# Kernel optimization log

Measured on AMD Instinct MI355X. Metric: run time of the kernel, lower is better.

## Reference

```python
import jax, jax.numpy as jnp
import numpy as np
import math

B, SV, ST, D, H = 16, 1024, 512, 768, 8
DH = D // H


def layernorm(x, g, b, eps=1e-5):
    m = jnp.mean(x, axis=-1, keepdims=True)
    v = jnp.var(x, axis=-1, keepdims=True)
    return (x - m) / jnp.sqrt(v + eps) * g + b


def setup_inputs() -> dict:
    key = jax.random.key(0)
    ks = jax.random.split(key, 12)
    s = 1.0 / math.sqrt(D)
    inp = {
        "visual_features": jax.random.normal(ks[0], (B, SV, D), jnp.float32),
        "text_features": jax.random.normal(ks[1], (B, ST, D), jnp.float32),
        "visual_mask": jnp.ones((B, SV), jnp.int32),
        "text_mask": jnp.ones((B, ST), jnp.int32),
        "Wq": jax.random.normal(ks[2], (D, D), jnp.float32) * s,
        "bq": jnp.zeros((D,), jnp.float32),
        "Wk": jax.random.normal(ks[3], (D, D), jnp.float32) * s,
        "bk": jnp.zeros((D,), jnp.float32),
        "Wv": jax.random.normal(ks[4], (D, D), jnp.float32) * s,
        "bv": jnp.zeros((D,), jnp.float32),
        "Wo": jax.random.normal(ks[5], (D, D), jnp.float32) * s,
        "bo": jnp.zeros((D,), jnp.float32),
        "ln1_g": jnp.ones((D,), jnp.float32),
        "ln1_b": jnp.zeros((D,), jnp.float32),
        "Wf": jax.random.normal(ks[6], (2 * D, D), jnp.float32) * (1.0 / math.sqrt(2 * D)),
        "bf": jnp.zeros((D,), jnp.float32),
        "ln2_g": jnp.ones((D,), jnp.float32),
        "ln2_b": jnp.zeros((D,), jnp.float32),
    }
    return inp


def _heads(x):
    b, s, _ = x.shape
    return x.reshape(b, s, H, DH)


def _cross_attn(q_feats, kv_feats, kv_mask, Wq, bq, Wk, bk, Wv, bv):
    # q_feats: [B,Sq,D], kv_feats: [B,Sk,D], kv_mask: [B,Sk] or None
    q = _heads(q_feats @ Wq + bq)   # [B,Sq,H,DH]
    k = _heads(kv_feats @ Wk + bk)  # [B,Sk,H,DH]
    v = _heads(kv_feats @ Wv + bv)
    scores = jnp.einsum('bqhd,bkhd->bhqk', q, k) / math.sqrt(DH)
    if kv_mask is not None:
        scores = jnp.where(kv_mask[:, None, None, :] == 0, -jnp.inf, scores)
    attn = jax.nn.softmax(scores, axis=-1)  # dropout is identity in eval
    out = jnp.einsum('bhqk,bkhd->bqhd', attn, v)
    return out.reshape(q_feats.shape[0], q_feats.shape[1], D)


def reference(visual_features, text_features, visual_mask, text_mask,
              Wq, bq, Wk, bk, Wv, bv, Wo, bo, ln1_g, ln1_b,
              Wf, bf, ln2_g, ln2_b):
    # visual queries attend to text
    v2t = _cross_attn(visual_features, text_features, text_mask, Wq, bq, Wk, bk, Wv, bv)
    # text queries attend to visual
    t2v = _cross_attn(text_features, visual_features, visual_mask, Wq, bq, Wk, bk, Wv, bv)
    attended_visual = layernorm(visual_features + (v2t @ Wo + bo), ln1_g, ln1_b)
    attended_text = layernorm(text_features + (t2v @ Wo + bo), ln1_g, ln1_b)
    # masked mean pooling
    vm = visual_mask[:, :, None].astype(jnp.float32)
    pooled_v = (attended_visual * vm).sum(1) / vm.sum(1)
    tm = text_mask[:, :, None].astype(jnp.float32)
    pooled_t = (attended_text * tm).sum(1) / tm.sum(1)
    fused = jnp.concatenate([pooled_v, pooled_t], axis=-1) @ Wf + bf
    fused = layernorm(fused, ln2_g, ln2_b)  # dropout identity in eval
    return fused
```

## Files before the change

kernel.cpp:

```cpp
#include <hip/hip_runtime.h>

typedef __bf16 bf16x8 __attribute__((ext_vector_type(8)));
typedef __bf16 bf16x4v __attribute__((ext_vector_type(4)));
typedef short s16x4 __attribute__((ext_vector_type(4)));
typedef float f32x4 __attribute__((ext_vector_type(4)));
typedef unsigned short u16;
typedef unsigned int u32;
typedef u16 u16x8 __attribute__((ext_vector_type(8)));
typedef u16 u16x4 __attribute__((ext_vector_type(4)));


__device__ __forceinline__ u16 f2bf(float f) {
    u32 u = __builtin_bit_cast(u32, f);
    u32 r = u + 0x7FFFu + ((u >> 16) & 1u);
    return (u16)(r >> 16);
}

__device__ __forceinline__ float bf2f(u16 b) {
    u32 u = ((u32)b) << 16;
    return __builtin_bit_cast(float, u);
}

__device__ __forceinline__ f32x4 mfma16(bf16x8 a, bf16x8 b, f32x4 c) {
    return __builtin_amdgcn_mfma_f32_16x16x32_bf16(a, b, c, 0, 0, 0);
}

__device__ __forceinline__ f32x4 mfma16k16(bf16x4v a, bf16x4v b, f32x4 c) {
#if __has_builtin(__builtin_amdgcn_mfma_f32_16x16x16_bf16)
    return __builtin_amdgcn_mfma_f32_16x16x16_bf16(a, b, c, 0, 0, 0);
#elif __has_builtin(__builtin_amdgcn_mfma_f32_16x16x16bf16_1k)
    return __builtin_amdgcn_mfma_f32_16x16x16bf16_1k(
        __builtin_bit_cast(s16x4, a), __builtin_bit_cast(s16x4, b), c, 0, 0, 0);
#else
    f32x4 d;
    asm volatile("v_mfma_f32_16x16x16_bf16 %0, %1, %2, %3"
                 : "=v"(d) : "v"(a), "v"(b), "v"(c));
    return d;
#endif
}

#define GLOAD_LDS16(g, l) __builtin_amdgcn_global_load_lds( \
    (__attribute__((address_space(1))) void*)(g), \
    (__attribute__((address_space(3))) void*)(l), 16, 0, 0)


__global__ __launch_bounds__(256) void k_cvt_x(const float* __restrict__ vf,
                                               const float* __restrict__ tf,
                                               u16* __restrict__ X, int nvis4) {
    int i = blockIdx.x * 256 + threadIdx.x;
    f32x4 v = (i < nvis4) ? ((const f32x4*)vf)[i] : ((const f32x4*)tf)[i - nvis4];
    u16x4 o = { f2bf(v[0]), f2bf(v[1]), f2bf(v[2]), f2bf(v[3]) };
    ((u16x4*)X)[i] = o;
}

__global__ __launch_bounds__(256) void k_transpose(const float* __restrict__ src,
                                                   u16* __restrict__ dst,
                                                   int K0, int N0) {
    __shared__ float t[64][65];
    int ntx = N0 >> 6;
    int k0 = (blockIdx.x / ntx) << 6, n0 = (blockIdx.x % ntx) << 6;
    int c = threadIdx.x & 63, rr = threadIdx.x >> 6;
#pragma unroll
    for (int q = 0; q < 16; q++) {
        int r = q * 4 + rr;
        t[r][c] = src[(size_t)(k0 + r) * N0 + n0 + c];
    }
    __syncthreads();
#pragma unroll
    for (int q = 0; q < 16; q++) {
        int r = q * 4 + rr;
        dst[(size_t)(n0 + r) * K0 + k0 + c] = f2bf(t[c][r]);
    }
}

__global__ __launch_bounds__(256) void k_bias(const float* __restrict__ bq,
                                              const float* __restrict__ bk,
                                              const float* __restrict__ bv,
                                              float* __restrict__ bqkv) {
    int n = blockIdx.x * 256 + threadIdx.x;
    if (n < 2304) {
        const float* s = (n < 768) ? bq : ((n < 1536) ? bk : bv);
        int r = (n < 768) ? n : ((n < 1536) ? n - 768 : n - 1536);
        bqkv[n] = s[r];
    }
}

__global__ __launch_bounds__(256) void k_zero(float* __restrict__ p) {
    p[blockIdx.x * 256 + threadIdx.x] = 0.f;
}

template <bool OUT_BF16, bool ADD_RES, bool SPLIT_VT>
__global__ __launch_bounds__(256) void k_gemm(const u16* __restrict__ A,
                                              const u16* __restrict__ Bt,
                                              const float* __restrict__ bias,
                                              const float* __restrict__ resA,
                                              const float* __restrict__ resB,
                                              void* __restrict__ Cout,
                                              int Ndim, int Kdim, int mvisL,
                                              u16* __restrict__ VtGp, int Rtot) {
    __shared__ alignas(16) u16 sA[2][128 * 32];
    __shared__ alignas(16) u16 sB[2][128 * 32];
    const int tid = threadIdx.x, wid = tid >> 6, lane = tid & 63;
    const int nwg = gridDim.x;
    const int wg = (blockIdx.x & 7) * (nwg >> 3) + (blockIdx.x >> 3);
    const int ntiles = Ndim >> 7;
    const int mt = wg / ntiles, nt = wg - mt * ntiles;
    const int m0 = mt << 7, n0 = nt << 7;
    const int wm = wid >> 1, wn = wid & 1;
    f32x4 acc[4][4] = {};

    const int r0 = tid >> 2, p0 = tid & 3;
    const int r1 = 64 + r0;
    const u16* ga0 = A + (size_t)(m0 + r0) * Kdim + p0 * 8;
    const u16* ga1 = A + (size_t)(m0 + r1) * Kdim + p0 * 8;
    const u16* gb0 = Bt + (size_t)(n0 + r0) * Kdim + p0 * 8;
    const u16* gb1 = Bt + (size_t)(n0 + r1) * Kdim + p0 * 8;
    const int loff0 = wid * 512;
    const int loff1 = 2048 + wid * 512;

    const int arow = (wm << 6) + (lane & 15);
    const int brow = (wn << 6) + (lane & 15);
    const int kg = (lane >> 4) * 8;

    auto stage = [&](int kt, int pb) {
        GLOAD_LDS16(ga0 + kt, &sA[pb][loff0]);
        GLOAD_LDS16(ga1 + kt, &sA[pb][loff1]);
        GLOAD_LDS16(gb0 + kt, &sB[pb][loff0]);
        GLOAD_LDS16(gb1 + kt, &sB[pb][loff1]);
    };

    const int niter = Kdim >> 5;
    stage(0, 0);
    for (int it = 0; it < niter; ++it) {
        const int cur = it & 1;
        __syncthreads();
        if (it + 1 < niter) stage((it + 1) << 5, cur ^ 1);
        bf16x8 av[4], bw[4];
#pragma unroll
        for (int i = 0; i < 4; i++) av[i] = *(const bf16x8*)&sA[cur][(arow + i * 16) * 32 + kg];
#pragma unroll
        for (int j = 0; j < 4; j++) bw[j] = *(const bf16x8*)&sB[cur][(brow + j * 16) * 32 + kg];
#pragma unroll
        for (int i = 0; i < 4; i++)
#pragma unroll
            for (int j = 0; j < 4; j++) acc[i][j] = mfma16(av[i], bw[j], acc[i][j]);
    }

    const int col0 = n0 + (wn << 6) + (lane & 15);
    const int rowb = m0 + (wm << 6) + ((lane >> 4) << 2);
    float bvals[4];
#pragma unroll
    for (int j = 0; j < 4; j++) bvals[j] = bias[col0 + j * 16];

    if constexpr (SPLIT_VT) {
        if (n0 >= 1536) {
            const int vcol0 = col0 - 1536;
#pragma unroll
            for (int i = 0; i < 4; i++) {
#pragma unroll
                for (int j = 0; j < 4; j++) {
                    u16x4 o4;
#pragma unroll
                    for (int rg = 0; rg < 4; rg++) o4[rg] = f2bf(acc[i][j][rg] + bvals[j]);
                    *(u16x4*)&VtGp[(size_t)(vcol0 + j * 16) * Rtot + rowb + i * 16] = o4;
                }
            }
            return;
        }
    }

#pragma unroll
    for (int i = 0; i < 4; i++) {
#pragma unroll
        for (int rg = 0; rg < 4; rg++) {
            const int row = rowb + i * 16 + rg;
            const float* rp = nullptr;
            if constexpr (ADD_RES)
                rp = (row < mvisL) ? resA + (size_t)row * 768
                                   : resB + (size_t)(row - mvisL) * 768;
#pragma unroll
            for (int j = 0; j < 4; j++) {
                const int col = col0 + j * 16;
                float v = acc[i][j][rg] + bvals[j];
                if constexpr (ADD_RES) v += rp[col];
                if constexpr (OUT_BF16)
                    ((u16*)Cout)[(size_t)row * Ndim + col] = f2bf(v);
                else
                    ((float*)Cout)[(size_t)row * Ndim + col] = v;
            }
        }
    }
}

__global__ __launch_bounds__(512) void k_attn(const u16* __restrict__ qkv,
                                              const u16* __restrict__ VtG,
                                              const int* __restrict__ vmaskc,
                                              const int* __restrict__ tmaskc,
                                              u16* __restrict__ attn, int CHn, int Rtot) {
    __shared__ alignas(16) u16 Kl[2][128 * 128];
    __shared__ alignas(16) u16 Vt[2][96 * 128];
    __shared__ float mk[2][128];

    const int bx = blockIdx.x;
    int b, h, qbase, kbase, nqt, ntl;
    const int* mask;
    const int vcap = CHn * 8;
    if (bx < vcap) {
        b = bx >> 3; h = bx & 7;
        qbase = b << 10; kbase = (CHn << 10) + (b << 9);
        mask = tmaskc + (b << 9); nqt = 4; ntl = 2;
    } else {
        const int bx2 = bx - vcap;
        b = bx2 >> 3; h = bx2 & 7;
        qbase = (CHn << 10) + (b << 9); kbase = b << 10;
        mask = vmaskc + (b << 10); nqt = 2; ntl = 3;
    }
    const int ntile = 1 << ntl;
    const int nsteps = nqt << ntl;
    const int tid = threadIdx.x, wid = tid >> 6, lane = tid & 63;
    const int l15 = lane & 15, l4 = lane >> 4;
    const float scale = 0.10206207261596577f;

    int koff[3];
#pragma unroll
    for (int kk = 0; kk < 3; kk++) koff[kk] = ((kk * 4 + l4) ^ (l15 & 7)) << 3;

    auto kt_of = [&](int s) {
        const int qt = s >> ntl, ktr = s & (ntile - 1);
        return (qt & 1) ? (ntile - 1 - ktr) : ktr;
    };
    auto stage = [&](int kt, int pb) {
#pragma unroll
        for (int it = 0; it < 4; ++it) {
            const int cb = it * 512 + (wid << 6);
            const int c = cb + lane;
            const int r = c >> 4, s8 = c & 15;
            const int k8 = s8 ^ (r & 7);
            const u16* src = qkv + (size_t)(kbase + (kt << 7) + r) * 2304 + 768 + h * 96
                             + (k8 < 12 ? k8 * 8 : 0);
            GLOAD_LDS16(src, &Kl[pb][(size_t)cb * 8]);
        }
#pragma unroll
        for (int it = 0; it < 3; ++it) {
            const int cb = it * 512 + (wid << 6);
            const int c = cb + lane;
            const int d = c >> 4, s8 = c & 15;
            const int k8 = s8 ^ (d & 7);
            const u16* src = VtG + (size_t)(h * 96 + d) * Rtot + kbase + (kt << 7) + k8 * 8;
            GLOAD_LDS16(src, &Vt[pb][(size_t)cb * 8]);
        }
        if (tid < 128) mk[pb][tid] = mask[(kt << 7) + tid] ? 0.f : -1e30f;
    };

    stage(kt_of(0), 0);
    int s = 0;
    for (int qt = 0; qt < nqt; ++qt) {
        bf16x8 aq[2][3];
#pragma unroll
        for (int qs = 0; qs < 2; ++qs) {
            const int qr = qbase + (qt << 8) + (wid << 5) + qs * 16 + l15;
#pragma unroll
            for (int kk = 0; kk < 3; kk++) {
                bf16x8 tq = *(const bf16x8*)&qkv[(size_t)qr * 2304 + h * 96 + kk * 32 + l4 * 8];
#pragma unroll
                for (int e = 0; e < 8; e++) tq[e] = (__bf16)((float)tq[e] * scale);
                aq[qs][kk] = tq;
            }
        }
        f32x4 o[2][6] = {};
        float mrunS[2] = {-1e30f, -1e30f};
        float lrunS[2] = {0.f, 0.f};

        for (int ktr = 0; ktr < ntile; ++ktr, ++s) {
            const int cur = s & 1;
            __syncthreads();
            if (s + 1 < nsteps) stage(kt_of(s + 1), cur ^ 1);

            f32x4 sc[2][8];
#pragma unroll
            for (int j = 0; j < 8; j++) {
                const int rbase = (j * 16 + l15) * 128;
                bf16x8 bk[3];
#pragma unroll
                for (int kk = 0; kk < 3; kk++)
                    bk[kk] = *(const bf16x8*)&Kl[cur][rbase + koff[kk]];
#pragma unroll
                for (int qs = 0; qs < 2; ++qs) {
                    f32x4 cj = {0.f, 0.f, 0.f, 0.f};
#pragma unroll
                    for (int kk = 0; kk < 3; kk++) cj = mfma16(bk[kk], aq[qs][kk], cj);
                    sc[qs][j] = cj;
                }
            }

            bf16x4v pb[2][8];
#pragma unroll
            for (int qs = 0; qs < 2; ++qs) {
                float tm = -1e30f;
#pragma unroll
                for (int j = 0; j < 8; j++) {
                    f32x4 m4 = *(const f32x4*)&mk[cur][j * 16 + (l4 << 2)];
#pragma unroll
                    for (int rg = 0; rg < 4; rg++) {
                        float v = sc[qs][j][rg] + m4[rg];
                        sc[qs][j][rg] = v;
                        tm = fmaxf(tm, v);
                    }
                }
                tm = fmaxf(tm, __shfl_xor(tm, 16));
                tm = fmaxf(tm, __shfl_xor(tm, 32));
                const int need = (tm > mrunS[qs] + 8.f) ? 1 : 0;
                if (__any(need)) {
                    float mn = fmaxf(mrunS[qs], tm);
                    float corrS = __expf(mrunS[qs] - mn);
                    mrunS[qs] = mn;
                    lrunS[qs] *= corrS;
                    float cr[4];
#pragma unroll
                    for (int rg = 0; rg < 4; rg++) cr[rg] = __shfl(corrS, (l4 << 2) + rg);
#pragma unroll
                    for (int j6 = 0; j6 < 6; j6++)
#pragma unroll
                        for (int rg = 0; rg < 4; rg++) o[qs][j6][rg] *= cr[rg];
                }
                float ts = 0.f;
#pragma unroll
                for (int j = 0; j < 8; j++) {
                    bf16x4v pq;
#pragma unroll
                    for (int rg = 0; rg < 4; rg++) {
                        float p = __expf(sc[qs][j][rg] - mrunS[qs]);
                        ts += p;
                        pq[rg] = (__bf16)p;
                    }
                    pb[qs][j] = pq;
                }
                ts += __shfl_xor(ts, 16);
                ts += __shfl_xor(ts, 32);
                lrunS[qs] += ts;
            }

#pragma unroll
            for (int j = 0; j < 8; j++) {
                const int slotb = 2 * j + (l4 >> 1);
                const int intra = (l4 & 1) << 2;
#pragma unroll
                for (int j6 = 0; j6 < 6; j6++) {
                    const int d = j6 * 16 + l15;
                    bf16x4v bv = *(const bf16x4v*)&Vt[cur][d * 128 +
                                     ((slotb ^ (l15 & 7)) << 3) + intra];
                    o[0][j6] = mfma16k16(pb[0][j], bv, o[0][j6]);
                    o[1][j6] = mfma16k16(pb[1][j], bv, o[1][j6]);
                }
            }
        }

#pragma unroll
        for (int qs = 0; qs < 2; ++qs) {
            const float invS = 1.f / lrunS[qs];
            float inv[4];
#pragma unroll
            for (int rg = 0; rg < 4; rg++) inv[rg] = __shfl(invS, (l4 << 2) + rg);
            const size_t orow = (size_t)(qbase + (qt << 8) + (wid << 5) + qs * 16);
#pragma unroll
            for (int j6 = 0; j6 < 6; j6++)
#pragma unroll
                for (int rg = 0; rg < 4; rg++)
                    attn[(orow + l4 * 4 + rg) * 768 + h * 96 + j6 * 16 + l15] =
                        f2bf(o[qs][j6][rg] * inv[rg]);
        }
    }
}

__global__ __launch_bounds__(256) void k_ln_pool(const u16* __restrict__ X,
                                                 const int* __restrict__ vmaskc,
                                                 const int* __restrict__ tmaskc,
                                                 const float* __restrict__ g,
                                                 const float* __restrict__ bb,
                                                 float* __restrict__ pooled,
                                                 int mvisL, int bg0) {
    __shared__ float pool[768];
    const int tid = threadIdx.x, wid = tid >> 6, lane = tid & 63;
    const int row0 = blockIdx.x << 5;
    const bool vis = row0 < mvisL;
    const int* mask = vis ? vmaskc : tmaskc;
    const int mbase = vis ? 0 : mvisL;
    const int bl = vis ? (row0 >> 10) : ((row0 - mvisL) >> 9);
    float* pout = pooled + (vis ? 0 : 12288) + (size_t)(bg0 + bl) * 768;

    float gv[12], bv2[12];
#pragma unroll
    for (int k = 0; k < 12; k++) { gv[k] = g[lane + k * 64]; bv2[k] = bb[lane + k * 64]; }
    float acc[12] = {};
    for (int rr = 0; rr < 8; ++rr) {
        const int row = row0 + (wid << 3) + rr;
        const u16* x = X + (size_t)row * 768;
        float xs[12], sm = 0.f, s2 = 0.f;
#pragma unroll
        for (int k = 0; k < 12; k++) {
            float tv = bf2f(x[lane + k * 64]);
            xs[k] = tv; sm += tv; s2 += tv * tv;
        }
#pragma unroll
        for (int d = 1; d < 64; d <<= 1) { sm += __shfl_xor(sm, d); s2 += __shfl_xor(s2, d); }
        const float mean = sm * (1.f / 768.f);
        const float rstd = rsqrtf(s2 * (1.f / 768.f) - mean * mean + 1e-5f);
        const float mv = (float)mask[row - mbase];
#pragma unroll
        for (int k = 0; k < 12; k++) acc[k] += ((xs[k] - mean) * rstd * gv[k] + bv2[k]) * mv;
    }
    pool[tid] = 0.f; pool[tid + 256] = 0.f; pool[tid + 512] = 0.f;
    __syncthreads();
#pragma unroll
    for (int k = 0; k < 12; k++) atomicAdd(&pool[lane + k * 64], acc[k]);
    __syncthreads();
    atomicAdd(&pout[tid], pool[tid]);
    atomicAdd(&pout[tid + 256], pool[tid + 256]);
    atomicAdd(&pout[tid + 512], pool[tid + 512]);
}

__device__ __forceinline__ float blk_sum(float v, volatile float* tmp) {
#pragma unroll
    for (int d = 1; d < 64; d <<= 1) v += __shfl_xor(v, d);
    __syncthreads();
    if ((threadIdx.x & 63) == 0) tmp[threadIdx.x >> 6] = v;
    __syncthreads();
    return tmp[0] + tmp[1] + tmp[2] + tmp[3];
}

__global__ __launch_bounds__(256) void k_final(const float* __restrict__ pooled,
                                               const int* __restrict__ vmask,
                                               const int* __restrict__ tmask,
                                               const float* __restrict__ Wf,
                                               const float* __restrict__ bfv,
                                               const float* __restrict__ g2,
                                               const float* __restrict__ b2,
                                               float* __restrict__ out) {
    __shared__ float sh[1536];
    __shared__ float red[4];
    const int b = blockIdx.x, tid = threadIdx.x;
    float cv = 0.f, ct = 0.f;
    for (int i = tid; i < 1024; i += 256) cv += (float)vmask[(b << 10) + i];
    for (int i = tid; i < 512; i += 256) ct += (float)tmask[(b << 9) + i];
    cv = blk_sum(cv, red);
    ct = blk_sum(ct, red);
    const float iv = 1.f / cv, itv = 1.f / ct;
#pragma unroll
    for (int k = 0; k < 3; k++) {
        int j = tid + (k << 8);
        sh[j] = pooled[b * 768 + j] * iv;
        sh[768 + j] = pooled[12288 + b * 768 + j] * itv;
    }
    __syncthreads();
    float f0 = bfv[tid], f1 = bfv[tid + 256], f2 = bfv[tid + 512];
    for (int i = 0; i < 1536; i++) {
        const float pv = sh[i];
        const float* w = Wf + (size_t)i * 768;
        f0 += pv * w[tid];
        f1 += pv * w[tid + 256];
        f2 += pv * w[tid + 512];
    }
    float sm = blk_sum(f0 + f1 + f2, red);
    float s2 = blk_sum(f0 * f0 + f1 * f1 + f2 * f2, red);
    const float mean = sm * (1.f / 768.f);
    const float rstd = rsqrtf(s2 * (1.f / 768.f) - mean * mean + 1e-5f);
    out[b * 768 + tid] = (f0 - mean) * rstd * g2[tid] + b2[tid];
    out[b * 768 + tid + 256] = (f1 - mean) * rstd * g2[tid + 256] + b2[tid + 256];
    out[b * 768 + tid + 512] = (f2 - mean) * rstd * g2[tid + 512] + b2[tid + 512];
}

extern "C" void kernel_launch(void* const* d_in, const int* in_sizes, int n_in,
                              void* d_out, int out_size, void* d_ws, size_t ws_size,
                              hipStream_t stream) {
    (void)in_sizes; (void)n_in; (void)out_size;
    const float* vf = (const float*)d_in[0];
    const float* tf = (const float*)d_in[1];
    const int* vmask = (const int*)d_in[2];
    const int* tmask = (const int*)d_in[3];
    const float* Wq = (const float*)d_in[4];
    const float* bq = (const float*)d_in[5];
    const float* Wk = (const float*)d_in[6];
    const float* bk = (const float*)d_in[7];
    const float* Wv = (const float*)d_in[8];
    const float* bv = (const float*)d_in[9];
    const float* Wo = (const float*)d_in[10];
    const float* bo = (const float*)d_in[11];
    const float* g1 = (const float*)d_in[12];
    const float* b1 = (const float*)d_in[13];
    const float* Wf = (const float*)d_in[14];
    const float* bfv = (const float*)d_in[15];
    const float* g2 = (const float*)d_in[16];
    const float* b2 = (const float*)d_in[17];
    float* outp = (float*)d_out;

    int CH = 16;
    while (CH > 1 && 4826112ull + (size_t)CH * 11796480ull > ws_size) CH >>= 1;
    const int NC = 16 / CH;
    const int Rtot = CH * 1536;

    char* ws = (char*)d_ws;
    u16*   wsW      = (u16*)(ws);
    u16*   wsWo     = (u16*)(ws + 3538944);
    float* wsBqkv   = (float*)(ws + 4718592);
    float* wsPooled = (float*)(ws + 4727808);
    u16*   wsX      = (u16*)(ws + 4826112);
    char*  qkvBase  = ws + 4826112 + (size_t)CH * 2359296;
    u16*   wsQKV    = (u16*)qkvBase;
    u16*   wsOproj  = (u16*)qkvBase;
    u16*   wsVtG    = (u16*)(qkvBase + (size_t)CH * 7077888);
    u16*   wsAttn   = wsX;

    k_transpose<<<dim3(144), dim3(256), 0, stream>>>(Wq, wsW, 768, 768);
    k_transpose<<<dim3(144), dim3(256), 0, stream>>>(Wk, wsW + 589824, 768, 768);
    k_transpose<<<dim3(144), dim3(256), 0, stream>>>(Wv, wsW + 1179648, 768, 768);
    k_transpose<<<dim3(144), dim3(256), 0, stream>>>(Wo, wsWo, 768, 768);
    k_bias<<<dim3(9), dim3(256), 0, stream>>>(bq, bk, bv, wsBqkv);
    k_zero<<<dim3(96), dim3(256), 0, stream>>>(wsPooled);

    for (int c = 0; c < NC; ++c) {
        const float* vfc = vf + (size_t)c * CH * 1024 * 768;
        const float* tfc = tf + (size_t)c * CH * 512 * 768;
        const int* vmc = vmask + c * CH * 1024;
        const int* tmc = tmask + c * CH * 512;

        k_cvt_x<<<dim3(CH * 1152), dim3(256), 0, stream>>>(vfc, tfc, wsX, CH * 196608);

        k_gemm<true, false, true><<<dim3(CH * 216), dim3(256), 0, stream>>>(
            wsX, wsW, wsBqkv, nullptr, nullptr, (void*)wsQKV, 2304, 768, 0, wsVtG, Rtot);

        k_attn<<<dim3(CH * 16), dim3(512), 0, stream>>>(
            wsQKV, wsVtG, vmc, tmc, wsAttn, CH, Rtot);

        k_gemm<true, true, false><<<dim3(CH * 72), dim3(256), 0, stream>>>(
            wsAttn, wsWo, bo, vfc, tfc, (void*)wsOproj, 768, 768, CH * 1024, nullptr, 0);

        k_ln_pool<<<dim3(CH * 48), dim3(256), 0, stream>>>(
            wsOproj, vmc, tmc, g1, b1, wsPooled, CH * 1024, c * CH);
    }

    k_final<<<dim3(16), dim3(256), 0, stream>>>(wsPooled, vmask, tmask, Wf, bfv, g2, b2, outp);
}
```

Measured before the change: 433.9 us.

## Enlarge GEMM tile to 256x128 with 512 threads and split final matvec across waves

The GEMM kernel moves from 128x128 tiles with 256 threads to 256x128 tiles with 512 threads (8 waves). The grid is halved and the A tile is staged as two 128-row halves, so each B tile is reused across twice as many rows. When the grid size is not a multiple of 8, the XCD-swizzle remapping is skipped. In the final fusion kernel, the 1536-long reduction is split across the 4 waves and combined through shared memory. The bigger tiles double LDS use and produce fewer workgroups, which may lower occupancy or leave the machine under-filled for small chunks.

```diff
diff --git a/kernel.cpp b/kernel.cpp
--- a/kernel.cpp
+++ b/kernel.cpp
@@ -90,7 +90,7 @@
 }
 
 template <bool OUT_BF16, bool ADD_RES, bool SPLIT_VT>
-__global__ __launch_bounds__(256) void k_gemm(const u16* __restrict__ A,
+__global__ __launch_bounds__(512) void k_gemm(const u16* __restrict__ A,
                                               const u16* __restrict__ Bt,
                                               const float* __restrict__ bias,
                                               const float* __restrict__ resA,
@@ -98,36 +98,35 @@
                                               void* __restrict__ Cout,
                                               int Ndim, int Kdim, int mvisL,
                                               u16* __restrict__ VtGp, int Rtot) {
-    __shared__ alignas(16) u16 sA[2][128 * 32];
+    __shared__ alignas(16) u16 sA[2][256 * 32];
     __shared__ alignas(16) u16 sB[2][128 * 32];
     const int tid = threadIdx.x, wid = tid >> 6, lane = tid & 63;
     const int nwg = gridDim.x;
-    const int wg = (blockIdx.x & 7) * (nwg >> 3) + (blockIdx.x >> 3);
+    const int wg = (nwg & 7) ? (int)blockIdx.x
+                             : ((blockIdx.x & 7) * (nwg >> 3) + (blockIdx.x >> 3));
     const int ntiles = Ndim >> 7;
     const int mt = wg / ntiles, nt = wg - mt * ntiles;
-    const int m0 = mt << 7, n0 = nt << 7;
+    const int m0 = mt << 8, n0 = nt << 7;
     const int wm = wid >> 1, wn = wid & 1;
     f32x4 acc[4][4] = {};
 
     const int r0 = tid >> 2, p0 = tid & 3;
-    const int r1 = 64 + r0;
-    const u16* ga0 = A + (size_t)(m0 + r0) * Kdim + p0 * 8;
-    const u16* ga1 = A + (size_t)(m0 + r1) * Kdim + p0 * 8;
-    const u16* gb0 = Bt + (size_t)(n0 + r0) * Kdim + p0 * 8;
-    const u16* gb1 = Bt + (size_t)(n0 + r1) * Kdim + p0 * 8;
-    const int loff0 = wid * 512;
-    const int loff1 = 2048 + wid * 512;
+    const u16* gaA0 = A + (size_t)(m0 + r0) * Kdim + p0 * 8;
+    const u16* gaA1 = A + (size_t)(m0 + 128 + r0) * Kdim + p0 * 8;
+    const u16* gaB  = Bt + (size_t)(n0 + r0) * Kdim + p0 * 8;
+    const int dA0 = (wid << 6) * 8;
+    const int dA1 = (512 + (wid << 6)) * 8;
+    const int dB  = (wid << 6) * 8;
+
+    auto stage = [&](int kt, int pb) {
+        GLOAD_LDS16(gaA0 + kt, &sA[pb][dA0]);
+        GLOAD_LDS16(gaA1 + kt, &sA[pb][dA1]);
+        GLOAD_LDS16(gaB + kt, &sB[pb][dB]);
+    };
 
     const int arow = (wm << 6) + (lane & 15);
     const int brow = (wn << 6) + (lane & 15);
     const int kg = (lane >> 4) * 8;
-
-    auto stage = [&](int kt, int pb) {
-        GLOAD_LDS16(ga0 + kt, &sA[pb][loff0]);
-        GLOAD_LDS16(ga1 + kt, &sA[pb][loff1]);
-        GLOAD_LDS16(gb0 + kt, &sB[pb][loff0]);
-        GLOAD_LDS16(gb1 + kt, &sB[pb][loff1]);
-    };
 
     const int niter = Kdim >> 5;
     stage(0, 0);
@@ -438,7 +437,9 @@
                                                float* __restrict__ out) {
     __shared__ float sh[1536];
     __shared__ float red[4];
+    __shared__ float pf[4][12][64];
     const int b = blockIdx.x, tid = threadIdx.x;
+    const int wid = tid >> 6, lane = tid & 63;
     float cv = 0.f, ct = 0.f;
     for (int i = tid; i < 1024; i += 256) cv += (float)vmask[(b << 10) + i];
     for (int i = tid; i < 512; i += 256) ct += (float)tmask[(b << 9) + i];
@@ -452,13 +453,22 @@
         sh[768 + j] = pooled[12288 + b * 768 + j] * itv;
     }
     __syncthreads();
+    float fp[12] = {};
+    for (int i = wid * 384; i < wid * 384 + 384; i++) {
+        const float pv = sh[i];
+        const float* w = Wf + (size_t)i * 768 + lane;
+#pragma unroll
+        for (int c = 0; c < 12; c++) fp[c] += pv * w[c * 64];
+    }
+#pragma unroll
+    for (int c = 0; c < 12; c++) pf[wid][c][lane] = fp[c];
+    __syncthreads();
     float f0 = bfv[tid], f1 = bfv[tid + 256], f2 = bfv[tid + 512];
-    for (int i = 0; i < 1536; i++) {
-        const float pv = sh[i];
-        const float* w = Wf + (size_t)i * 768;
-        f0 += pv * w[tid];
-        f1 += pv * w[tid + 256];
-        f2 += pv * w[tid + 512];
+#pragma unroll
+    for (int w4 = 0; w4 < 4; w4++) {
+        f0 += pf[w4][wid][lane];
+        f1 += pf[w4][wid + 4][lane];
+        f2 += pf[w4][wid + 8][lane];
     }
     float sm = blk_sum(f0 + f1 + f2, red);
     float s2 = blk_sum(f0 * f0 + f1 * f1 + f2 * f2, red);
@@ -525,13 +535,13 @@
 
         k_cvt_x<<<dim3(CH * 1152), dim3(256), 0, stream>>>(vfc, tfc, wsX, CH * 196608);
 
-        k_gemm<true, false, true><<<dim3(CH * 216), dim3(256), 0, stream>>>(
+        k_gemm<true, false, true><<<dim3(CH * 108), dim3(512), 0, stream>>>(
             wsX, wsW, wsBqkv, nullptr, nullptr, (void*)wsQKV, 2304, 768, 0, wsVtG, Rtot);
 
         k_attn<<<dim3(CH * 16), dim3(512), 0, stream>>>(
             wsQKV, wsVtG, vmc, tmc, wsAttn, CH, Rtot);
 
-        k_gemm<true, true, false><<<dim3(CH * 72), dim3(256), 0, stream>>>(
+        k_gemm<true, true, false><<<dim3(CH * 36), dim3(512), 0, stream>>>(
             wsAttn, wsWo, bo, vfc, tfc, (void*)wsOproj, 768, 768, CH * 1024, nullptr, 0);
 
         k_ln_pool<<<dim3(CH * 48), dim3(256), 0, stream>>>(
```

New measurement: 380.2 us, median of 3. 1.14x faster.
